# Kernel optimization log

Hardware: AMD Instinct MI355X
Metric: run time of the kernel (lower is better)

Reference implementation:

```python
import jax, jax.numpy as jnp
import numpy as np

N_NODES = 100000
N_EDGES = 1600000
N_GRAPHS = 128
K_HOPS = 3  # TAGConv default K
HIDDEN = 128
IN_FEAT = 4
NUM_CLASSES = 2


def setup_inputs() -> dict:
    key = jax.random.key(0)
    ks = jax.random.split(key, 10)
    x = jax.random.normal(ks[0], (N_NODES, IN_FEAT), dtype=jnp.float32)
    W1 = jax.random.normal(ks[1], (K_HOPS + 1, IN_FEAT, HIDDEN), dtype=jnp.float32) * 0.1
    b1 = jax.random.normal(ks[2], (HIDDEN,), dtype=jnp.float32) * 0.1
    W2 = jax.random.normal(ks[3], (K_HOPS + 1, HIDDEN, HIDDEN), dtype=jnp.float32) * 0.1
    b2 = jax.random.normal(ks[4], (HIDDEN,), dtype=jnp.float32) * 0.1
    Wlin = jax.random.normal(ks[5], (HIDDEN, NUM_CLASSES), dtype=jnp.float32) * 0.1
    blin = jax.random.normal(ks[6], (NUM_CLASSES,), dtype=jnp.float32) * 0.1
    edge_index = jax.random.randint(ks[7], (2, N_EDGES), 0, N_NODES, dtype=jnp.int32)
    batch = jnp.sort(jax.random.randint(ks[8], (N_NODES,), 0, N_GRAPHS, dtype=jnp.int32))
    return {"x": x, "W1": W1, "b1": b1, "W2": W2, "b2": b2,
            "Wlin": Wlin, "blin": blin, "edge_index": edge_index, "batch": batch}


def _gcn_norm(edge_index, num_nodes):
    # symmetric normalization, no self-loops (TAGConv: add_self_loops=False)
    row, col = edge_index[0], edge_index[1]
    ones = jnp.ones((edge_index.shape[1],), dtype=jnp.float32)
    deg = jax.ops.segment_sum(ones, col, num_segments=num_nodes)
    dinv = jnp.where(deg > 0, jax.lax.rsqrt(jnp.maximum(deg, 1.0)), 0.0)
    return dinv[row] * dinv[col]  # [E]


def _tagconv(x, row, col, norm, W, b):
    # out = sum_k (A_norm^k x) @ W[k] + b
    out = x @ W[0]
    h = x
    for k in range(1, W.shape[0]):
        h = jax.ops.segment_sum(h[row] * norm[:, None], col, num_segments=x.shape[0])
        out = out + h @ W[k]
    return out + b


def reference(x, W1, b1, W2, b2, Wlin, blin, edge_index, batch):
    row, col = edge_index[0], edge_index[1]
    norm = _gcn_norm(edge_index, x.shape[0])
    h = jax.nn.relu(_tagconv(x, row, col, norm, W1, b1))
    h = jax.nn.relu(_tagconv(h, row, col, norm, W2, b2))
    # global mean pool over graphs
    sums = jax.ops.segment_sum(h, batch, num_segments=N_GRAPHS)
    cnts = jax.ops.segment_sum(jnp.ones((h.shape[0],), dtype=h.dtype), batch, num_segments=N_GRAPHS)
    pooled = sums / jnp.maximum(cnts, 1.0)[:, None]
    # dropout is identity in eval mode
    logits = pooled @ Wlin + blin
    return jax.nn.softmax(logits, axis=-1)
```

## Files before the change

kernel.cpp:

```cpp
#include <hip/hip_runtime.h>

#define NNODES 100000
#define NEDGES 1600000
#define NGRAPHS 128
#define HID 128
#define NBKT 782
#define NPAD  (NBKT * 128)
#define CHUNK 8192
#define NCHB ((NEDGES + CHUNK - 1) / CHUNK)
#define MAXB 3072

typedef unsigned short ushort_t;
typedef unsigned int uint_t;
typedef __attribute__((ext_vector_type(8))) short short8;
typedef __attribute__((ext_vector_type(4))) float floatx4;

__device__ __forceinline__ float bf2f(ushort_t u) {
    return __uint_as_float(((unsigned)u) << 16);
}
__device__ __forceinline__ ushort_t f2bf(float f) {
    unsigned u = __float_as_uint(f);
    return (ushort_t)((u + 0x7fffu + ((u >> 16) & 1u)) >> 16);
}

__global__ void hist_k(const int* __restrict__ col, int* __restrict__ bcnt) {
    __shared__ int l[NBKT];
    for (int i = threadIdx.x; i < NBKT; i += 256) l[i] = 0;
    __syncthreads();
    int base = blockIdx.x * CHUNK;
    int lim = base + CHUNK < NEDGES ? base + CHUNK : NEDGES;
    for (int e = base + threadIdx.x; e < lim; e += 256)
        atomicAdd(&l[col[e] >> 7], 1);
    __syncthreads();
    for (int i = threadIdx.x; i < NBKT; i += 256)
        if (l[i]) atomicAdd(&bcnt[i], l[i]);
}

__global__ void bscan_k(const int* __restrict__ bcnt, int* __restrict__ bbase,
                        int* __restrict__ gc) {
    __shared__ int l[1024];
    int t = threadIdx.x;
    int v0 = (t < NBKT) ? bcnt[t] : 0;
    l[t] = v0;
    __syncthreads();
    for (int d = 1; d < 1024; d <<= 1) {
        int v = (t >= d) ? l[t - d] : 0;
        __syncthreads();
        l[t] += v;
        __syncthreads();
    }
    if (t < NBKT) { int ex = l[t] - v0; bbase[t] = ex; gc[t] = ex; }
    if (t == 0) bbase[NBKT] = NEDGES;
}

__global__ void bfill_k(const int* __restrict__ row, const int* __restrict__ col,
                        int* __restrict__ gc, uint_t* __restrict__ entry) {
    __shared__ int lcnt[NBKT], lbase[NBKT];
    for (int i = threadIdx.x; i < NBKT; i += 256) lcnt[i] = 0;
    __syncthreads();
    int base = blockIdx.x * CHUNK;
    int lim = base + CHUNK < NEDGES ? base + CHUNK : NEDGES;
    for (int e = base + threadIdx.x; e < lim; e += 256)
        atomicAdd(&lcnt[col[e] >> 7], 1);
    __syncthreads();
    for (int i = threadIdx.x; i < NBKT; i += 256) {
        int c = lcnt[i];
        lbase[i] = c ? atomicAdd(&gc[i], c) : 0;
        lcnt[i] = 0;
    }
    __syncthreads();
    for (int e = base + threadIdx.x; e < lim; e += 256) {
        int c = col[e];
        int b = c >> 7;
        int pos = lbase[b] + atomicAdd(&lcnt[b], 1);
        entry[pos] = (uint_t)row[e] | ((uint_t)(c & 127) << 17);
    }
}

__global__ void sortb_k(const uint_t* __restrict__ entry, const int* __restrict__ bbase,
                        int* __restrict__ csr_src, int* __restrict__ degi,
                        int* __restrict__ off) {
    __shared__ uint_t ents[MAXB];
    __shared__ uint_t sorted[MAXB];
    __shared__ int ncnt[128], nsc[128], nfill[128];
    int b = blockIdx.x;
    int base = bbase[b];
    int cnt = bbase[b + 1] - base;
    if (cnt > MAXB) cnt = MAXB;
    int t = threadIdx.x;
    if (t < 128) { ncnt[t] = 0; nfill[t] = 0; }
    __syncthreads();
    for (int i = t; i < cnt; i += 256) {
        uint_t v = entry[base + i];
        ents[i] = v;
        atomicAdd(&ncnt[v >> 17], 1);
    }
    __syncthreads();
    if (t < 128) nsc[t] = ncnt[t];
    __syncthreads();
    for (int d = 1; d < 128; d <<= 1) {
        int v = (t >= d && t < 128) ? nsc[t - d] : 0;
        __syncthreads();
        if (t < 128) nsc[t] += v;
        __syncthreads();
    }
    if (t < 128) {
        int n = b * 128 + t;
        if (n < NNODES) { degi[n] = ncnt[t]; off[n] = base + nsc[t]; }
        nsc[t] -= ncnt[t];
    }
    __syncthreads();
    for (int i = t; i < cnt; i += 256) {
        uint_t v = ents[i];
        int dl = v >> 17;
        int pos = nsc[dl] + atomicAdd(&nfill[dl], 1);
        sorted[pos] = v & 0x1FFFFu;
    }
    __syncthreads();
    for (int i = t; i < cnt; i += 256) csr_src[base + i] = (int)sorted[i];
}

__global__ void misc_k(const int* __restrict__ degi, float* __restrict__ dinv,
                       const float* __restrict__ W2, ushort_t* __restrict__ Wt,
                       const int* __restrict__ batch,
                       int* __restrict__ first, int* __restrict__ last) {
    int i = blockIdx.x * 256 + threadIdx.x;
    if (i < NNODES) {
        int d = degi[i];
        dinv[i] = (d > 0) ? rsqrtf((float)d) : 0.0f;
        int g = batch[i];
        if (i == 0 || batch[i - 1] != g) first[g] = i;
        if (i == NNODES - 1 || batch[i + 1] != g) last[g] = i;
    }
    if (i < 512 * 128) {
        int j = i >> 9, k = i & 511;
        Wt[i] = f2bf(W2[k * 128 + j]);
    }
}

__global__ void wfill_k(const int* __restrict__ off, const int* __restrict__ csr_src,
                        const float* __restrict__ dinv, uint2* __restrict__ epk) {
    int n = blockIdx.x * 256 + threadIdx.x;
    if (n >= NNODES) return;
    int k = n ? off[n - 1] : 0;
    int end = off[n];
    float dn = dinv[n];
    for (; k < end; k++) {
        int s = csr_src[k];
        epk[k] = make_uint2((uint_t)s, __float_as_uint(dinv[s] * dn));
    }
}

__global__ void gprop4(const int* __restrict__ off, const uint2* __restrict__ epk,
                       const float* __restrict__ hin, float* __restrict__ hout) {
    int n = blockIdx.x * 256 + threadIdx.x;
    if (n >= NNODES) return;
    int k = n ? off[n - 1] : 0;
    int end = off[n];
    float4 acc = {0.f, 0.f, 0.f, 0.f};
    for (; k + 3 < end; k += 4) {
        uint2 e0 = epk[k], e1 = epk[k + 1], e2 = epk[k + 2], e3 = epk[k + 3];
        float w0 = __uint_as_float(e0.y), w1 = __uint_as_float(e1.y);
        float w2 = __uint_as_float(e2.y), w3 = __uint_as_float(e3.y);
        float4 v0 = *(const float4*)(hin + e0.x * 4);
        float4 v1 = *(const float4*)(hin + e1.x * 4);
        float4 v2 = *(const float4*)(hin + e2.x * 4);
        float4 v3 = *(const float4*)(hin + e3.x * 4);
        acc.x += w0 * v0.x + w1 * v1.x + w2 * v2.x + w3 * v3.x;
        acc.y += w0 * v0.y + w1 * v1.y + w2 * v2.y + w3 * v3.y;
        acc.z += w0 * v0.z + w1 * v1.z + w2 * v2.z + w3 * v3.z;
        acc.w += w0 * v0.w + w1 * v1.w + w2 * v2.w + w3 * v3.w;
    }
    for (; k < end; k++) {
        uint2 e = epk[k];
        float w = __uint_as_float(e.y);
        float4 v = *(const float4*)(hin + e.x * 4);
        acc.x += w * v.x; acc.y += w * v.y; acc.z += w * v.z; acc.w += w * v.w;
    }
    *(float4*)(hout + n * 4) = acc;
}

__device__ __forceinline__ void acc8(float* a, float wgt, uint4 v) {
    a[0] += wgt * __uint_as_float(v.x << 16);
    a[1] += wgt * __uint_as_float(v.x & 0xffff0000u);
    a[2] += wgt * __uint_as_float(v.y << 16);
    a[3] += wgt * __uint_as_float(v.y & 0xffff0000u);
    a[4] += wgt * __uint_as_float(v.z << 16);
    a[5] += wgt * __uint_as_float(v.z & 0xffff0000u);
    a[6] += wgt * __uint_as_float(v.w << 16);
    a[7] += wgt * __uint_as_float(v.w & 0xffff0000u);
}

__global__ void gprop128(const int* __restrict__ off, const uint2* __restrict__ epk,
                         const ushort_t* __restrict__ hin, ushort_t* __restrict__ hout) {
    int t = blockIdx.x * 256 + threadIdx.x;
    int n = t >> 4, lane = t & 15;
    if (n >= NNODES) return;
    int k = n ? off[n - 1] : 0;
    int end = off[n];
    int fo = lane * 8;
    float a[8] = {0.f, 0.f, 0.f, 0.f, 0.f, 0.f, 0.f, 0.f};
    for (; k + 3 < end; k += 4) {
        uint2 e0 = epk[k], e1 = epk[k + 1], e2 = epk[k + 2], e3 = epk[k + 3];
        uint4 v0 = *(const uint4*)(hin + e0.x * HID + fo);
        uint4 v1 = *(const uint4*)(hin + e1.x * HID + fo);
        uint4 v2 = *(const uint4*)(hin + e2.x * HID + fo);
        uint4 v3 = *(const uint4*)(hin + e3.x * HID + fo);
        acc8(a, __uint_as_float(e0.y), v0);
        acc8(a, __uint_as_float(e1.y), v1);
        acc8(a, __uint_as_float(e2.y), v2);
        acc8(a, __uint_as_float(e3.y), v3);
    }
    for (; k < end; k++) {
        uint2 e = epk[k];
        uint4 v = *(const uint4*)(hin + e.x * HID + fo);
        acc8(a, __uint_as_float(e.y), v);
    }
    uint4 o;
    o.x = (unsigned)f2bf(a[0]) | ((unsigned)f2bf(a[1]) << 16);
    o.y = (unsigned)f2bf(a[2]) | ((unsigned)f2bf(a[3]) << 16);
    o.z = (unsigned)f2bf(a[4]) | ((unsigned)f2bf(a[5]) << 16);
    o.w = (unsigned)f2bf(a[6]) | ((unsigned)f2bf(a[7]) << 16);
    *(uint4*)(hout + n * HID + fo) = o;
}

__global__ void combine1(const float* __restrict__ x, const float* __restrict__ h1,
                         const float* __restrict__ h2, const float* __restrict__ h3,
                         const float* __restrict__ W1, const float* __restrict__ b1,
                         ushort_t* __restrict__ P0) {
    __shared__ float hs[4][16];
    int n0 = blockIdx.x * 4;
    int j = threadIdx.x;
    if (j < 64) {
        int n = j >> 4, v = j & 15, k = v >> 2, i = v & 3;
        const float* src = (k == 0) ? x : (k == 1) ? h1 : (k == 2) ? h2 : h3;
        hs[n][v] = src[(n0 + n) * 4 + i];
    }
    __syncthreads();
    float w[16];
#pragma unroll
    for (int v = 0; v < 16; v++) w[v] = W1[v * 128 + j];
    float bb = b1[j];
#pragma unroll
    for (int n = 0; n < 4; n++) {
        float acc = bb;
#pragma unroll
        for (int v = 0; v < 16; v++) acc += hs[n][v] * w[v];
        P0[(n0 + n) * 128 + j] = f2bf(fmaxf(acc, 0.0f));
    }
}

__global__ __launch_bounds__(256) void gemm4p(
    const ushort_t* __restrict__ P0, const ushort_t* __restrict__ P1,
    const ushort_t* __restrict__ P2, const ushort_t* __restrict__ P3,
    const ushort_t* __restrict__ Wt, const float* __restrict__ b2,
    const int* __restrict__ batch, float* __restrict__ sums) {
    __shared__ ushort_t Bs[32768];
    int tid = threadIdx.x;
    int w = tid >> 6, lane = tid & 63;
    int r16 = lane & 15, kg = lane >> 4;
    int tb = blockIdx.x * 128 + w * 32;
    bool active = (tb < NNODES);
    floatx4 acc[2][8];
#pragma unroll
    for (int s = 0; s < 2; s++)
#pragma unroll
        for (int n = 0; n < 8; n++) acc[s][n] = (floatx4){0.f, 0.f, 0.f, 0.f};
    const ushort_t* Ps[4] = {P0, P1, P2, P3};
    for (int stage = 0; stage < 2; stage++) {
        __syncthreads();
#pragma unroll
        for (int i = 0; i < 16; i++) {
            int idx = i * 256 + tid;
            int r = idx >> 5;
            int slot = idx & 31;
            int cb = (slot * 16) ^ ((r & 7) << 4);
            *(uint4*)((char*)Bs + r * 512 + cb) =
                *(const uint4*)(Wt + r * 512 + stage * 256 + slot * 8);
        }
        __syncthreads();
        if (active) {
#pragma unroll
            for (int hh = 0; hh < 2; hh++) {
                const ushort_t* P = Ps[stage * 2 + hh];
#pragma unroll
                for (int k0 = 0; k0 < 128; k0 += 32) {
                    int f = k0 + kg * 8;
                    short8 a0 = *(const short8*)(P + (tb + r16) * HID + f);
                    short8 a1 = *(const short8*)(P + (tb + 16 + r16) * HID + f);
#pragma unroll
                    for (int n = 0; n < 8; n++) {
                        int r = n * 16 + r16;
                        int cb = (hh * 256 + k0 * 2 + kg * 16) ^ ((r & 7) << 4);
                        short8 b = *(const short8*)((const char*)Bs + r * 512 + cb);
                        acc[0][n] = __builtin_amdgcn_mfma_f32_16x16x32_bf16(a0, b, acc[0][n], 0, 0, 0);
                        acc[1][n] = __builtin_amdgcn_mfma_f32_16x16x32_bf16(a1, b, acc[1][n], 0, 0, 0);
                    }
                }
            }
        }
    }
    if (!active) return;
    float bb[8];
#pragma unroll
    for (int n = 0; n < 8; n++) bb[n] = b2[n * 16 + r16];
    int g0 = batch[tb], g31 = batch[tb + 31];
    if (g0 == g31) {
#pragma unroll
        for (int n = 0; n < 8; n++) {
            float s = 0.0f;
#pragma unroll
            for (int st = 0; st < 2; st++)
#pragma unroll
                for (int r = 0; r < 4; r++) s += fmaxf(acc[st][n][r] + bb[n], 0.0f);
            s += __shfl_xor(s, 16);
            s += __shfl_xor(s, 32);
            if (kg == 0) atomicAdd(&sums[g0 * HID + n * 16 + r16], s);
        }
    } else {
#pragma unroll
        for (int st = 0; st < 2; st++)
#pragma unroll
            for (int r = 0; r < 4; r++) {
                int g = batch[tb + st * 16 + kg * 4 + r];
#pragma unroll
                for (int n = 0; n < 8; n++)
                    atomicAdd(&sums[g * HID + n * 16 + r16], fmaxf(acc[st][n][r] + bb[n], 0.0f));
            }
    }
}

__global__ void head_kernel(const float* __restrict__ sums, const int* __restrict__ first,
                            const int* __restrict__ last,
                            const float* __restrict__ Wlin, const float* __restrict__ blin,
                            float* __restrict__ out) {
    int g = threadIdx.x;
    if (g >= NGRAPHS) return;
    float cnt = (float)(last[g] - first[g] + 1);
    if (cnt < 1.0f) cnt = 1.0f;
    float l0 = blin[0], l1 = blin[1];
    for (int i = 0; i < HID; i++) {
        float p = sums[g * HID + i] / cnt;
        l0 += p * Wlin[i * 2 + 0];
        l1 += p * Wlin[i * 2 + 1];
    }
    float m = fmaxf(l0, l1);
    float e0 = __expf(l0 - m), e1 = __expf(l1 - m);
    float s = e0 + e1;
    out[g * 2 + 0] = e0 / s;
    out[g * 2 + 1] = e1 / s;
}

#define OFF_DINV  0
#define OFF_DEGI  (OFF_DINV + NPAD)
#define OFF_OFF   (OFF_DEGI + NPAD)
#define OFF_SUMS  (OFF_OFF + NPAD)
#define OFF_FIRST (OFF_SUMS + NGRAPHS * HID)
#define OFF_LAST  (OFF_FIRST + NGRAPHS)
#define OFF_BCNT  (OFF_LAST + NGRAPHS)
#define ZERO_WORDS (NGRAPHS * HID + NGRAPHS + NGRAPHS + 800)
#define OFF_BBASE (OFF_BCNT + 800)
#define OFF_GC    (OFF_BBASE + 800)
#define OFF_ENT   (OFF_GC + 800)
#define OFF_SRC   (OFF_ENT + NEDGES)
#define OFF_EPK   (OFF_SRC + NEDGES)
#define OFF_P0    (OFF_EPK + 2 * NEDGES)
#define OFF_P1    (OFF_P0 + NNODES * HID / 2)
#define OFF_P2    (OFF_P1 + NNODES * HID / 2)
#define OFF_P3    (OFF_P2 + NNODES * HID / 2)
#define OFF_H1    (OFF_P3 + NNODES * HID / 2)
#define OFF_H2    (OFF_H1 + NNODES * 4)
#define OFF_H3    (OFF_H2 + NNODES * 4)
#define OFF_WT    (OFF_H3 + NNODES * 4)

extern "C" void kernel_launch(void* const* d_in, const int* in_sizes, int n_in,
                              void* d_out, int out_size, void* d_ws, size_t ws_size,
                              hipStream_t stream) {
    const float* x    = (const float*)d_in[0];
    const float* W1   = (const float*)d_in[1];
    const float* b1   = (const float*)d_in[2];
    const float* W2   = (const float*)d_in[3];
    const float* b2   = (const float*)d_in[4];
    const float* Wlin = (const float*)d_in[5];
    const float* blin = (const float*)d_in[6];
    const int* ei     = (const int*)d_in[7];
    const int* batch  = (const int*)d_in[8];
    float* out = (float*)d_out;

    const int* row = ei;
    const int* col = ei + NEDGES;

    float* ws = (float*)d_ws;
    float* dinv    = ws + OFF_DINV;
    int*   degi    = (int*)(ws + OFF_DEGI);
    int*   off     = (int*)(ws + OFF_OFF);
    float* sums    = ws + OFF_SUMS;
    int*   first   = (int*)(ws + OFF_FIRST);
    int*   last    = (int*)(ws + OFF_LAST);
    int*   bcnt    = (int*)(ws + OFF_BCNT);
    int*   bbase   = (int*)(ws + OFF_BBASE);
    int*   gc      = (int*)(ws + OFF_GC);
    uint_t* ent    = (uint_t*)(ws + OFF_ENT);
    int*   csr_src = (int*)(ws + OFF_SRC);
    uint2* epk     = (uint2*)(ws + OFF_EPK);
    ushort_t* P0   = (ushort_t*)(ws + OFF_P0);
    ushort_t* P1   = (ushort_t*)(ws + OFF_P1);
    ushort_t* P2   = (ushort_t*)(ws + OFF_P2);
    ushort_t* P3   = (ushort_t*)(ws + OFF_P3);
    float* h1      = ws + OFF_H1;
    float* h2      = ws + OFF_H2;
    float* h3      = ws + OFF_H3;
    ushort_t* Wt   = (ushort_t*)(ws + OFF_WT);

    hipMemsetAsync(sums, 0, ZERO_WORDS * sizeof(float), stream);

    hist_k<<<NCHB, 256, 0, stream>>>(col, bcnt);
    bscan_k<<<1, 1024, 0, stream>>>(bcnt, bbase, gc);
    bfill_k<<<NCHB, 256, 0, stream>>>(row, col, gc, ent);
    sortb_k<<<NBKT, 256, 0, stream>>>(ent, bbase, csr_src, degi, off);
    misc_k<<<NPAD / 256, 256, 0, stream>>>(degi, dinv, W2, Wt, batch, first, last);
    wfill_k<<<NPAD / 256, 256, 0, stream>>>(off, csr_src, dinv, epk);

    gprop4<<<NPAD / 256, 256, 0, stream>>>(off, epk, x, h1);
    gprop4<<<NPAD / 256, 256, 0, stream>>>(off, epk, h1, h2);
    gprop4<<<NPAD / 256, 256, 0, stream>>>(off, epk, h2, h3);
    combine1<<<NNODES / 4, 128, 0, stream>>>(x, h1, h2, h3, W1, b1, P0);

    gprop128<<<NPAD * 16 / 256, 256, 0, stream>>>(off, epk, P0, P1);
    gprop128<<<NPAD * 16 / 256, 256, 0, stream>>>(off, epk, P1, P2);
    gprop128<<<NPAD * 16 / 256, 256, 0, stream>>>(off, epk, P2, P3);

    gemm4p<<<(NNODES + 127) / 128, 256, 0, stream>>>(P0, P1, P2, P3, Wt, b2, batch, sums);

    head_kernel<<<1, 128, 0, stream>>>(sums, first, last, Wlin, blin, out);
}
```

Baseline: 362.4 us.

## Slice 128-wide features into 8 feature slabs for cache-local gather propagation

Node features are stored as 8 slabs of 16 bf16 features each, with every slab covering all nodes. The propagation kernel now handles one slab per block, using 2 threads per node, so each gather pass touches a 3.2MB working set that fits in cache instead of the full 25MB matrix. Edge-list reads and output stores use nontemporal hints to avoid polluting the cache. The cost is that each edge list is re-read 8 times, and combine1 and the GEMM A-loads are adjusted to the slab layout.

```diff
diff --git a/kernel.cpp b/kernel.cpp
--- a/kernel.cpp
+++ b/kernel.cpp
@@ -9,11 +9,15 @@
 #define CHUNK 8192
 #define NCHB ((NEDGES + CHUNK - 1) / CHUNK)
 #define MAXB 3072
+#define NSL 8
+#define SLS (NPAD * 16)
 
 typedef unsigned short ushort_t;
 typedef unsigned int uint_t;
+typedef unsigned long long u64;
 typedef __attribute__((ext_vector_type(8))) short short8;
 typedef __attribute__((ext_vector_type(4))) float floatx4;
+typedef __attribute__((ext_vector_type(4))) unsigned int uint4e;
 
 __device__ __forceinline__ float bf2f(ushort_t u) {
     return __uint_as_float(((unsigned)u) << 16);
@@ -191,37 +195,44 @@
     a[7] += wgt * __uint_as_float(v.w & 0xffff0000u);
 }
 
-__global__ void gprop128(const int* __restrict__ off, const uint2* __restrict__ epk,
-                         const ushort_t* __restrict__ hin, ushort_t* __restrict__ hout) {
-    int t = blockIdx.x * 256 + threadIdx.x;
-    int n = t >> 4, lane = t & 15;
+__global__ void gprop128s(const int* __restrict__ off, const uint2* __restrict__ epk,
+                          const ushort_t* __restrict__ Pin, ushort_t* __restrict__ Pout) {
+    int s = blockIdx.x & 7;
+    int nb = blockIdx.x >> 3;
+    int n = nb * 128 + (threadIdx.x >> 1);
     if (n >= NNODES) return;
+    int lane = threadIdx.x & 1;
     int k = n ? off[n - 1] : 0;
     int end = off[n];
+    const ushort_t* Ps_ = Pin + (size_t)s * SLS;
     int fo = lane * 8;
     float a[8] = {0.f, 0.f, 0.f, 0.f, 0.f, 0.f, 0.f, 0.f};
+    const u64* ep = (const u64*)epk;
     for (; k + 3 < end; k += 4) {
-        uint2 e0 = epk[k], e1 = epk[k + 1], e2 = epk[k + 2], e3 = epk[k + 3];
-        uint4 v0 = *(const uint4*)(hin + e0.x * HID + fo);
-        uint4 v1 = *(const uint4*)(hin + e1.x * HID + fo);
-        uint4 v2 = *(const uint4*)(hin + e2.x * HID + fo);
-        uint4 v3 = *(const uint4*)(hin + e3.x * HID + fo);
-        acc8(a, __uint_as_float(e0.y), v0);
-        acc8(a, __uint_as_float(e1.y), v1);
-        acc8(a, __uint_as_float(e2.y), v2);
-        acc8(a, __uint_as_float(e3.y), v3);
+        u64 e0 = __builtin_nontemporal_load(ep + k);
+        u64 e1 = __builtin_nontemporal_load(ep + k + 1);
+        u64 e2 = __builtin_nontemporal_load(ep + k + 2);
+        u64 e3 = __builtin_nontemporal_load(ep + k + 3);
+        uint4 v0 = *(const uint4*)(Ps_ + (uint_t)(e0 & 0xffffffffu) * 16 + fo);
+        uint4 v1 = *(const uint4*)(Ps_ + (uint_t)(e1 & 0xffffffffu) * 16 + fo);
+        uint4 v2 = *(const uint4*)(Ps_ + (uint_t)(e2 & 0xffffffffu) * 16 + fo);
+        uint4 v3 = *(const uint4*)(Ps_ + (uint_t)(e3 & 0xffffffffu) * 16 + fo);
+        acc8(a, __uint_as_float((uint_t)(e0 >> 32)), v0);
+        acc8(a, __uint_as_float((uint_t)(e1 >> 32)), v1);
+        acc8(a, __uint_as_float((uint_t)(e2 >> 32)), v2);
+        acc8(a, __uint_as_float((uint_t)(e3 >> 32)), v3);
     }
     for (; k < end; k++) {
-        uint2 e = epk[k];
-        uint4 v = *(const uint4*)(hin + e.x * HID + fo);
-        acc8(a, __uint_as_float(e.y), v);
-    }
-    uint4 o;
+        u64 e = __builtin_nontemporal_load(ep + k);
+        uint4 v = *(const uint4*)(Ps_ + (uint_t)(e & 0xffffffffu) * 16 + fo);
+        acc8(a, __uint_as_float((uint_t)(e >> 32)), v);
+    }
+    uint4e o;
     o.x = (unsigned)f2bf(a[0]) | ((unsigned)f2bf(a[1]) << 16);
     o.y = (unsigned)f2bf(a[2]) | ((unsigned)f2bf(a[3]) << 16);
     o.z = (unsigned)f2bf(a[4]) | ((unsigned)f2bf(a[5]) << 16);
     o.w = (unsigned)f2bf(a[6]) | ((unsigned)f2bf(a[7]) << 16);
-    *(uint4*)(hout + n * HID + fo) = o;
+    __builtin_nontemporal_store(o, (uint4e*)(Pout + (size_t)s * SLS + (size_t)n * 16 + fo));
 }
 
 __global__ void combine1(const float* __restrict__ x, const float* __restrict__ h1,
@@ -241,12 +252,13 @@
 #pragma unroll
     for (int v = 0; v < 16; v++) w[v] = W1[v * 128 + j];
     float bb = b1[j];
+    int sbase = (j >> 4) * SLS + (j & 15);
 #pragma unroll
     for (int n = 0; n < 4; n++) {
         float acc = bb;
 #pragma unroll
         for (int v = 0; v < 16; v++) acc += hs[n][v] * w[v];
-        P0[(n0 + n) * 128 + j] = f2bf(fmaxf(acc, 0.0f));
+        P0[sbase + (n0 + n) * 16] = f2bf(fmaxf(acc, 0.0f));
     }
 }
 
@@ -286,8 +298,9 @@
 #pragma unroll
                 for (int k0 = 0; k0 < 128; k0 += 32) {
                     int f = k0 + kg * 8;
-                    short8 a0 = *(const short8*)(P + (tb + r16) * HID + f);
-                    short8 a1 = *(const short8*)(P + (tb + 16 + r16) * HID + f);
+                    const ushort_t* Pa = P + (f >> 4) * SLS + (f & 15);
+                    short8 a0 = *(const short8*)(Pa + (tb + r16) * 16);
+                    short8 a1 = *(const short8*)(Pa + (tb + 16 + r16) * 16);
 #pragma unroll
                     for (int n = 0; n < 8; n++) {
                         int r = n * 16 + r16;
@@ -364,11 +377,12 @@
 #define OFF_ENT   (OFF_GC + 800)
 #define OFF_SRC   (OFF_ENT + NEDGES)
 #define OFF_EPK   (OFF_SRC + NEDGES)
+#define PSZ       (NPAD * HID / 2)
 #define OFF_P0    (OFF_EPK + 2 * NEDGES)
-#define OFF_P1    (OFF_P0 + NNODES * HID / 2)
-#define OFF_P2    (OFF_P1 + NNODES * HID / 2)
-#define OFF_P3    (OFF_P2 + NNODES * HID / 2)
-#define OFF_H1    (OFF_P3 + NNODES * HID / 2)
+#define OFF_P1    (OFF_P0 + PSZ)
+#define OFF_P2    (OFF_P1 + PSZ)
+#define OFF_P3    (OFF_P2 + PSZ)
+#define OFF_H1    (OFF_P3 + PSZ)
 #define OFF_H2    (OFF_H1 + NNODES * 4)
 #define OFF_H3    (OFF_H2 + NNODES * 4)
 #define OFF_WT    (OFF_H3 + NNODES * 4)
@@ -426,9 +440,9 @@
     gprop4<<<NPAD / 256, 256, 0, stream>>>(off, epk, h2, h3);
     combine1<<<NNODES / 4, 128, 0, stream>>>(x, h1, h2, h3, W1, b1, P0);
 
-    gprop128<<<NPAD * 16 / 256, 256, 0, stream>>>(off, epk, P0, P1);
-    gprop128<<<NPAD * 16 / 256, 256, 0, stream>>>(off, epk, P1, P2);
-    gprop128<<<NPAD * 16 / 256, 256, 0, stream>>>(off, epk, P2, P3);
+    gprop128s<<<NBKT * NSL, 256, 0, stream>>>(off, epk, P0, P1);
+    gprop128s<<<NBKT * NSL, 256, 0, stream>>>(off, epk, P1, P2);
+    gprop128s<<<NBKT * NSL, 256, 0, stream>>>(off, epk, P2, P3);
 
     gemm4p<<<(NNODES + 127) / 128, 256, 0, stream>>>(P0, P1, P2, P3, Wt, b2, batch, sums);
 
```

New measurement: 766.4 us. 2.12x slower.
